# Performance work log

Measured on AMD Instinct MI355X. Metric: run time of the kernel, lower is better.

Reference implementation:

```python
import jax, jax.numpy as jnp
import numpy as np

N_NODES = 50000
N_EDGES = 1600000
IN_FEAT = 128
OUT_FEAT = 128
NUM_RELS = 16
NUM_BASES = 4


def setup_inputs() -> dict:
    key = jax.random.key(0)
    ks = jax.random.split(key, 7)
    x = jax.random.normal(ks[0], (N_NODES, IN_FEAT), dtype=jnp.float32)
    W_bases = jax.random.normal(ks[1], (NUM_BASES, IN_FEAT, OUT_FEAT), dtype=jnp.float32) * (1.0 / np.sqrt(IN_FEAT))
    w_comp = jax.random.normal(ks[2], (NUM_RELS, NUM_BASES), dtype=jnp.float32)
    norm = jax.random.uniform(ks[3], (N_EDGES, 1), dtype=jnp.float32)
    src = jax.random.randint(ks[4], (N_EDGES,), 0, N_NODES, dtype=jnp.int32)
    dst = jax.random.randint(ks[5], (N_EDGES,), 0, N_NODES, dtype=jnp.int32)
    etype = jax.random.randint(ks[6], (N_EDGES,), 0, NUM_RELS, dtype=jnp.int32)
    return {"x": x, "W_bases": W_bases, "w_comp": w_comp, "norm": norm,
            "src": src, "dst": dst, "etype": etype}


def _combine_weights(W_bases, w_comp):
    # Faithful to the torch code: stack -> permute(1,0,2) -> matmul -> view(-1, out) -> split(in_feat)
    # [B, in, out] -> [in, B, out]
    Wb = jnp.transpose(W_bases, (1, 0, 2))
    # [R, B] @ [in, B, out] (batched over 'in') -> [in, R, out]
    W = jnp.matmul(w_comp, Wb)
    # view(-1, out) then split into chunks of in_feat rows == reshape(R, in, out)
    return W.reshape(-1, OUT_FEAT).reshape(NUM_RELS, IN_FEAT, OUT_FEAT)


def reference(x, W_bases, w_comp, norm, src, dst, etype):
    # per-relation weights [R, in, out]
    W = _combine_weights(W_bases, w_comp)
    # src_mul_edge: gather source node features, scale by per-edge norm  [E, in]
    msg = x[src] * norm
    # 'sum' aggregation per (relation, dst-node) segment  -> [R, N, in]
    seg = etype.astype(jnp.int32) * N_NODES + dst.astype(jnp.int32)
    agg = jax.ops.segment_sum(msg, seg, num_segments=NUM_RELS * N_NODES)
    agg = agg.reshape(NUM_RELS, N_NODES, IN_FEAT)
    # per-relation mm then merge across relation subgraphs with node_reduce 'sum'  -> [N, out]
    out = jnp.einsum('rni,rio->no', agg, W)
    # bias=None, activation=None in this configuration
    return out
```

## Files before the change

kernel.cpp:

```cpp
#include <hip/hip_runtime.h>


#define N_NODES  50000
#define N_EDGES  1600000
#define IN_FEAT  128
#define OUT_FEAT 128
#define NUM_RELS 16
#define NUM_BASES 4
#define XC_K     32
#define BIN_CAP  96

#define OFF_CNT      0
#define OFF_SPILLCNT 200000
#define OFF_SPILL    200064
#define OFF_BINS     6600064
#define OFF_XC       45000064
#define WS_NEED      51400064

__global__ __launch_bounds__(256) void node_precomp(
    const float* __restrict__ x, const float* __restrict__ w_comp,
    float* __restrict__ xc)
{
  const int lane = threadIdx.x & 31;
  const int grp  = threadIdx.x >> 5;
  const int j = lane & 7;
  const int b = lane >> 3;

  float wc[16];
  #pragma unroll
  for (int t = 0; t < 16; ++t) wc[t] = w_comp[t * NUM_BASES + b];

  for (int n = blockIdx.x * 8 + grp; n < N_NODES; n += gridDim.x * 8) {
    const float4* xr = (const float4*)(x + (size_t)n * IN_FEAT) + j * 4;
    float acc = 0.f;
    #pragma unroll
    for (int q = 0; q < 4; ++q) {
      float4 v = xr[q];
      acc += v.x * wc[q*4+0] + v.y * wc[q*4+1]
           + v.z * wc[q*4+2] + v.w * wc[q*4+3];
    }
    xc[(size_t)n * XC_K + lane] = acc;
  }
}

__global__ __launch_bounds__(256) void bin_edges(
    const int* __restrict__ src, const int* __restrict__ dst,
    const int* __restrict__ etype, const float* __restrict__ norm,
    int* __restrict__ cnt, uint2* __restrict__ bins,
    int* __restrict__ spillcnt, int* __restrict__ spill)
{
  for (int e = blockIdx.x * blockDim.x + threadIdx.x; e < N_EDGES;
       e += gridDim.x * blockDim.x) {
    const int d  = dst[e];
    const int s  = src[e];
    const int et = etype[e];
    const float nm = norm[e];
    const int pos = atomicAdd(&cnt[d], 1);
    if (pos < BIN_CAP) {
      bins[(size_t)d * BIN_CAP + pos] =
          make_uint2((unsigned)s | ((unsigned)et << 17), __float_as_uint(nm));
    } else {
      const int k = atomicAdd(spillcnt, 1);
      if (k < N_EDGES) spill[k] = e;
    }
  }
}

__global__ __launch_bounds__(512) void rgcn_fused(
    const int* __restrict__ cnt, const uint2* __restrict__ bins,
    const float* __restrict__ xc, const float* __restrict__ Wb,
    float* __restrict__ out)
{
  __shared__ float acc[8 * 1024];

  const int t    = threadIdx.x;
  const int w    = t >> 6;
  const int lane = t & 63;
  const int h    = lane >> 5;
  const int l5   = lane & 31;
  const int jj4b = (l5 & 7) * 4 + (l5 >> 3);
  const int accBase = w * 1024 + h * 512;

  const int nodeBase = blockIdx.x * 8;
  const int n = nodeBase + w;

  #pragma unroll
  for (int q = 0; q < 4; ++q)
    *(float4*)&acc[w * 1024 + lane * 16 + q * 4] = make_float4(0.f,0.f,0.f,0.f);

  int cntv = 0;
  uint32_t B0x = 0, B0y = 0, B1x = 0, B1y = 0;
  if (n < N_NODES) {
    cntv = cnt[n]; if (cntv > BIN_CAP) cntv = BIN_CAP;
    const uint2* bp = bins + (size_t)n * BIN_CAP;
    uint2 v0 = bp[lane];  B0x = v0.x; B0y = v0.y;
    uint2 v1 = bp[(lane & 31) + 64]; B1x = v1.x; B1y = v1.y;
  }

  const int iters = (cntv + 1) >> 1;
  int   idx  = h;
  bool  act0 = idx < cntv;
  uint32_t wx = (idx < 64) ? __shfl(B0x, idx) : __shfl(B1x, (idx - 64) & 31);
  uint32_t wy = (idx < 64) ? __shfl(B0y, idx) : __shfl(B1y, (idx - 64) & 31);
  int   s0  = wx & 0x1FFFF;
  int   et0 = (wx >> 17) & 15;
  float nm0 = __uint_as_float(wy);
  float xc0 = act0 ? xc[(size_t)s0 * XC_K + l5] : 0.f;

  for (int i = 0; i < iters; ++i) {
    const int idx1 = 2 * (i + 1) + h;
    const bool act1 = idx1 < cntv;
    uint32_t nx = (idx1 < 64) ? __shfl(B0x, idx1) : __shfl(B1x, (idx1 - 64) & 31);
    uint32_t ny = (idx1 < 64) ? __shfl(B0y, idx1) : __shfl(B1y, (idx1 - 64) & 31);
    const int   s1  = nx & 0x1FFFF;
    const int   et1 = (nx >> 17) & 15;
    const float nm1 = __uint_as_float(ny);
    const float xc1 = act1 ? xc[(size_t)s1 * XC_K + l5] : 0.f;
    if (act0) {
      const int slot = accBase + et0 * 32 + jj4b;
      acc[slot] += xc0 * nm0;
    }
    act0 = act1; xc0 = xc1; et0 = et1; nm0 = nm1;
  }

  #pragma unroll
  for (int q = 0; q < 8; ++q) {
    const int idxm = w * 1024 + q * 64 + lane;
    acc[idxm] += acc[idxm + 512];
  }
  __syncthreads();

  const int o  = t & 127;
  const int g  = t >> 7;
  const float* a0p = &acc[(2 * g) * 1024];
  const float* a1p = &acc[(2 * g + 1) * 1024];
  const float* wp0 = Wb + o;
  float o0 = 0.f, o1 = 0.f;
  #pragma unroll 4
  for (int m = 0; m < 128; ++m) {
    const float4 a0 = *(const float4*)&a0p[m * 4];
    const float4 a1 = *(const float4*)&a1p[m * 4];
    const float w0 = wp0[(m          ) * 128];
    const float w1 = wp0[(m + 128    ) * 128];
    const float w2 = wp0[(m + 256    ) * 128];
    const float w3 = wp0[(m + 384    ) * 128];
    o0 += a0.x * w0 + a0.y * w1 + a0.z * w2 + a0.w * w3;
    o1 += a1.x * w0 + a1.y * w1 + a1.z * w2 + a1.w * w3;
  }
  const int n0 = nodeBase + 2 * g;
  const int n1 = n0 + 1;
  if (n0 < N_NODES) out[(size_t)n0 * OUT_FEAT + o] = o0;
  if (n1 < N_NODES) out[(size_t)n1 * OUT_FEAT + o] = o1;
}

__global__ __launch_bounds__(256) void spill_fix(
    const int* __restrict__ spillcnt, const int* __restrict__ spill,
    const float* __restrict__ xc, const float* __restrict__ Wb,
    const float* __restrict__ norm, const int* __restrict__ src,
    const int* __restrict__ dst, const int* __restrict__ etype,
    float* __restrict__ out)
{
  int cntv = *spillcnt; if (cntv > N_EDGES) cntv = N_EDGES;
  for (int idx = blockIdx.x * blockDim.x + threadIdx.x; idx < cntv;
       idx += gridDim.x * blockDim.x) {
    const int e = spill[idx];
    const int s = src[e], d = dst[e], et = etype[e];
    const float nm = norm[e];
    float m[32];
    #pragma unroll
    for (int l = 0; l < 32; ++l) m[l] = xc[(size_t)s * XC_K + l] * nm;
    for (int o = 0; o < OUT_FEAT; ++o) {
      float a = 0.f;
      #pragma unroll
      for (int l = 0; l < 32; ++l)
        a += m[l] * Wb[(size_t)((l >> 3) * 128 + et * 8 + (l & 7)) * OUT_FEAT + o];
      atomicAdd(&out[(size_t)d * OUT_FEAT + o], a);
    }
  }
}

__global__ __launch_bounds__(256) void edge_direct(
    const float* __restrict__ x, const float* __restrict__ W_bases,
    const float* __restrict__ w_comp, const float* __restrict__ norm,
    const int* __restrict__ src, const int* __restrict__ dst,
    const int* __restrict__ etype, float* __restrict__ out)
{
  const int wave = threadIdx.x >> 6;
  const int lane = threadIdx.x & 63;
  const int j = lane & 7;
  const int b = (lane >> 3) & 3;

  float wc[16];
  #pragma unroll
  for (int t = 0; t < 16; ++t) wc[t] = w_comp[t * NUM_BASES + b];

  for (int e = blockIdx.x * 4 + wave; e < N_EDGES; e += gridDim.x * 4) {
    const int   s  = src[e];
    const int   d  = dst[e];
    const int   et = etype[e];
    const float nm = norm[e];
    const float4* xr = (const float4*)(x + (size_t)s * IN_FEAT) + j * 4;
    float m = 0.f;
    #pragma unroll
    for (int q = 0; q < 4; ++q) {
      float4 v = xr[q];
      m += v.x * wc[q*4+0] + v.y * wc[q*4+1]
         + v.z * wc[q*4+2] + v.w * wc[q*4+3];
    }
    m *= nm;
    float acc0 = 0.f, acc1 = 0.f;
    #pragma unroll
    for (int p = 0; p < 32; ++p) {
      float mv = __shfl(m, p, 64);
      const float* Wr = W_bases + (size_t)((p >> 3) * 128 + et * 8 + (p & 7)) * OUT_FEAT;
      acc0 += mv * Wr[lane];
      acc1 += mv * Wr[64 + lane];
    }
    atomicAdd(out + (size_t)d * OUT_FEAT + lane, acc0);
    atomicAdd(out + (size_t)d * OUT_FEAT + 64 + lane, acc1);
  }
}

extern "C" void kernel_launch(void* const* d_in, const int* in_sizes, int n_in,
                              void* d_out, int out_size, void* d_ws, size_t ws_size,
                              hipStream_t stream) {
  const float* x       = (const float*)d_in[0];
  const float* W_bases = (const float*)d_in[1];
  const float* w_comp  = (const float*)d_in[2];
  const float* norm    = (const float*)d_in[3];
  const int*   src     = (const int*)d_in[4];
  const int*   dst     = (const int*)d_in[5];
  const int*   etype   = (const int*)d_in[6];
  float* out = (float*)d_out;

  if (ws_size >= (size_t)WS_NEED) {
    char* ws = (char*)d_ws;
    int*   cntp     = (int*)(ws + OFF_CNT);
    int*   spillcnt = (int*)(ws + OFF_SPILLCNT);
    int*   spill    = (int*)(ws + OFF_SPILL);
    uint2* bins     = (uint2*)(ws + OFF_BINS);
    float* xc       = (float*)(ws + OFF_XC);

    hipMemsetAsync(cntp, 0, 200064, stream);
    node_precomp<<<6250, 256, 0, stream>>>(x, w_comp, xc);
    bin_edges<<<6250, 256, 0, stream>>>(src, dst, etype, norm,
                                        cntp, bins, spillcnt, spill);
    rgcn_fused<<<(N_NODES + 7) / 8, 512, 0, stream>>>(cntp, bins, xc, W_bases, out);
    spill_fix<<<16, 256, 0, stream>>>(spillcnt, spill, xc, W_bases,
                                      norm, src, dst, etype, out);
  } else {
    hipMemsetAsync(out, 0, (size_t)out_size * sizeof(float), stream);
    edge_direct<<<8192, 256, 0, stream>>>(x, W_bases, w_comp, norm,
                                          src, dst, etype, out);
  }
}
```

Measured before the change: 461.2 us.

## Fuse prep kernels and register-tile the per-node weight GEMM in rgcn_fused

Merges node precompute and edge binning into one launch, with vectorized int4 loads for the edge arrays. The fused kernel now handles 16 nodes per block with LDS atomic accumulation and a transposed padded layout. The output GEMM is register-tiled (4 nodes by 8 outputs per thread, split-K across waves with an LDS tree reduction), so each W element is reused across nodes instead of reloaded per node. Risks include LDS atomic contention, extra barriers, and no bounds checks on nodes, which relies on N_NODES being divisible by 16.

```diff
diff --git a/kernel.cpp b/kernel.cpp
--- a/kernel.cpp
+++ b/kernel.cpp
@@ -9,6 +9,8 @@
 #define NUM_BASES 4
 #define XC_K     32
 #define BIN_CAP  96
+#define NPB      16
+#define ASTRIDE  20
 
 #define OFF_CNT      0
 #define OFF_SPILLCNT 200000
@@ -17,140 +19,190 @@
 #define OFF_XC       45000064
 #define WS_NEED      51400064
 
-__global__ __launch_bounds__(256) void node_precomp(
+__global__ __launch_bounds__(256) void prep(
     const float* __restrict__ x, const float* __restrict__ w_comp,
-    float* __restrict__ xc)
-{
-  const int lane = threadIdx.x & 31;
-  const int grp  = threadIdx.x >> 5;
-  const int j = lane & 7;
-  const int b = lane >> 3;
-
-  float wc[16];
-  #pragma unroll
-  for (int t = 0; t < 16; ++t) wc[t] = w_comp[t * NUM_BASES + b];
-
-  for (int n = blockIdx.x * 8 + grp; n < N_NODES; n += gridDim.x * 8) {
-    const float4* xr = (const float4*)(x + (size_t)n * IN_FEAT) + j * 4;
-    float acc = 0.f;
-    #pragma unroll
-    for (int q = 0; q < 4; ++q) {
-      float4 v = xr[q];
-      acc += v.x * wc[q*4+0] + v.y * wc[q*4+1]
-           + v.z * wc[q*4+2] + v.w * wc[q*4+3];
-    }
-    xc[(size_t)n * XC_K + lane] = acc;
-  }
-}
-
-__global__ __launch_bounds__(256) void bin_edges(
     const int* __restrict__ src, const int* __restrict__ dst,
     const int* __restrict__ etype, const float* __restrict__ norm,
-    int* __restrict__ cnt, uint2* __restrict__ bins,
+    float* __restrict__ xc, int* __restrict__ cnt, uint2* __restrict__ bins,
     int* __restrict__ spillcnt, int* __restrict__ spill)
 {
-  for (int e = blockIdx.x * blockDim.x + threadIdx.x; e < N_EDGES;
-       e += gridDim.x * blockDim.x) {
-    const int d  = dst[e];
-    const int s  = src[e];
-    const int et = etype[e];
-    const float nm = norm[e];
-    const int pos = atomicAdd(&cnt[d], 1);
-    if (pos < BIN_CAP) {
-      bins[(size_t)d * BIN_CAP + pos] =
-          make_uint2((unsigned)s | ((unsigned)et << 17), __float_as_uint(nm));
-    } else {
-      const int k = atomicAdd(spillcnt, 1);
-      if (k < N_EDGES) spill[k] = e;
-    }
-  }
-}
-
-__global__ __launch_bounds__(512) void rgcn_fused(
+  if (blockIdx.x < 512) {
+    const int lane = threadIdx.x & 31;
+    const int grp  = threadIdx.x >> 5;
+    const int j = lane & 7;
+    const int b = lane >> 3;
+    float wc[16];
+    #pragma unroll
+    for (int t = 0; t < 16; ++t) wc[t] = w_comp[t * NUM_BASES + b];
+    for (int n = blockIdx.x * 8 + grp; n < N_NODES; n += 512 * 8) {
+      const float4* xr = (const float4*)(x + (size_t)n * IN_FEAT) + j * 4;
+      float acc = 0.f;
+      #pragma unroll
+      for (int q = 0; q < 4; ++q) {
+        float4 v = xr[q];
+        acc += v.x * wc[q*4+0] + v.y * wc[q*4+1]
+             + v.z * wc[q*4+2] + v.w * wc[q*4+3];
+      }
+      xc[n * XC_K + lane] = acc;
+    }
+  } else {
+    const int bid = blockIdx.x - 512;
+    for (int e4 = (bid * 256 + threadIdx.x) * 4; e4 < N_EDGES;
+         e4 += 1536 * 256 * 4) {
+      const int4   s4 = *(const int4*)&src[e4];
+      const int4   d4 = *(const int4*)&dst[e4];
+      const int4   t4 = *(const int4*)&etype[e4];
+      const float4 n4 = *(const float4*)&norm[e4];
+      const int   ss[4] = {s4.x, s4.y, s4.z, s4.w};
+      const int   dd[4] = {d4.x, d4.y, d4.z, d4.w};
+      const int   tt[4] = {t4.x, t4.y, t4.z, t4.w};
+      const float nn[4] = {n4.x, n4.y, n4.z, n4.w};
+      #pragma unroll
+      for (int q = 0; q < 4; ++q) {
+        const int pos = atomicAdd(&cnt[dd[q]], 1);
+        if (pos < BIN_CAP) {
+          bins[(size_t)dd[q] * BIN_CAP + pos] =
+              make_uint2((unsigned)ss[q] | ((unsigned)tt[q] << 17),
+                         __float_as_uint(nn[q]));
+        } else {
+          const int k = atomicAdd(spillcnt, 1);
+          if (k < N_EDGES) spill[k] = e4 + q;
+        }
+      }
+    }
+  }
+}
+
+__device__ inline void red_write(float* accf, int slot, float4 (&ac)[4][2]) {
+  const int base = slot * 34;
+  #pragma unroll
+  for (int nn = 0; nn < 4; ++nn) {
+    *(float2*)&accf[base + nn*8 + 0] = make_float2(ac[nn][0].x, ac[nn][0].y);
+    *(float2*)&accf[base + nn*8 + 2] = make_float2(ac[nn][0].z, ac[nn][0].w);
+    *(float2*)&accf[base + nn*8 + 4] = make_float2(ac[nn][1].x, ac[nn][1].y);
+    *(float2*)&accf[base + nn*8 + 6] = make_float2(ac[nn][1].z, ac[nn][1].w);
+  }
+}
+__device__ inline void red_read(const float* accf, int slot, float4 (&ac)[4][2]) {
+  const int base = slot * 34;
+  #pragma unroll
+  for (int nn = 0; nn < 4; ++nn) {
+    float2 v0 = *(const float2*)&accf[base + nn*8 + 0];
+    float2 v1 = *(const float2*)&accf[base + nn*8 + 2];
+    float2 v2 = *(const float2*)&accf[base + nn*8 + 4];
+    float2 v3 = *(const float2*)&accf[base + nn*8 + 6];
+    ac[nn][0].x += v0.x; ac[nn][0].y += v0.y;
+    ac[nn][0].z += v1.x; ac[nn][0].w += v1.y;
+    ac[nn][1].x += v2.x; ac[nn][1].y += v2.y;
+    ac[nn][1].z += v3.x; ac[nn][1].w += v3.y;
+  }
+}
+
+__global__ __launch_bounds__(512, 4) void rgcn_fused(
     const int* __restrict__ cnt, const uint2* __restrict__ bins,
     const float* __restrict__ xc, const float* __restrict__ Wb,
     float* __restrict__ out)
 {
-  __shared__ float acc[8 * 1024];
+  __shared__ float accf[512 * ASTRIDE];
 
   const int t    = threadIdx.x;
   const int w    = t >> 6;
   const int lane = t & 63;
   const int h    = lane >> 5;
   const int l5   = lane & 31;
-  const int jj4b = (l5 & 7) * 4 + (l5 >> 3);
-  const int accBase = w * 1024 + h * 512;
-
-  const int nodeBase = blockIdx.x * 8;
-  const int n = nodeBase + w;
-
-  #pragma unroll
-  for (int q = 0; q < 4; ++q)
-    *(float4*)&acc[w * 1024 + lane * 16 + q * 4] = make_float4(0.f,0.f,0.f,0.f);
-
-  int cntv = 0;
-  uint32_t B0x = 0, B0y = 0, B1x = 0, B1y = 0;
-  if (n < N_NODES) {
-    cntv = cnt[n]; if (cntv > BIN_CAP) cntv = BIN_CAP;
-    const uint2* bp = bins + (size_t)n * BIN_CAP;
-    uint2 v0 = bp[lane];  B0x = v0.x; B0y = v0.y;
-    uint2 v1 = bp[(lane & 31) + 64]; B1x = v1.x; B1y = v1.y;
-  }
-
-  const int iters = (cntv + 1) >> 1;
-  int   idx  = h;
-  bool  act0 = idx < cntv;
-  uint32_t wx = (idx < 64) ? __shfl(B0x, idx) : __shfl(B1x, (idx - 64) & 31);
-  uint32_t wy = (idx < 64) ? __shfl(B0y, idx) : __shfl(B1y, (idx - 64) & 31);
-  int   s0  = wx & 0x1FFFF;
-  int   et0 = (wx >> 17) & 15;
-  float nm0 = __uint_as_float(wy);
-  float xc0 = act0 ? xc[(size_t)s0 * XC_K + l5] : 0.f;
-
-  for (int i = 0; i < iters; ++i) {
-    const int idx1 = 2 * (i + 1) + h;
-    const bool act1 = idx1 < cntv;
-    uint32_t nx = (idx1 < 64) ? __shfl(B0x, idx1) : __shfl(B1x, (idx1 - 64) & 31);
-    uint32_t ny = (idx1 < 64) ? __shfl(B0y, idx1) : __shfl(B1y, (idx1 - 64) & 31);
-    const int   s1  = nx & 0x1FFFF;
-    const int   et1 = (nx >> 17) & 15;
-    const float nm1 = __uint_as_float(ny);
-    const float xc1 = act1 ? xc[(size_t)s1 * XC_K + l5] : 0.f;
-    if (act0) {
-      const int slot = accBase + et0 * 32 + jj4b;
-      acc[slot] += xc0 * nm0;
-    }
-    act0 = act1; xc0 = xc1; et0 = et1; nm0 = nm1;
-  }
-
-  #pragma unroll
-  for (int q = 0; q < 8; ++q) {
-    const int idxm = w * 1024 + q * 64 + lane;
-    acc[idxm] += acc[idxm + 512];
-  }
-  __syncthreads();
-
-  const int o  = t & 127;
-  const int g  = t >> 7;
-  const float* a0p = &acc[(2 * g) * 1024];
-  const float* a1p = &acc[(2 * g + 1) * 1024];
-  const float* wp0 = Wb + o;
-  float o0 = 0.f, o1 = 0.f;
+  const int perm = (l5 & 7) * 4 + (l5 >> 3);
+
+  #pragma unroll
+  for (int i = 0; i < 5; ++i)
+    *(float4*)&accf[t * ASTRIDE + i * 4] = make_float4(0.f, 0.f, 0.f, 0.f);
+  __syncthreads();
+
+  const int nodeBase = blockIdx.x * NPB;
+  const int n0g = nodeBase + 2 * w;
+  const int n1g = n0g + 1;
+  int c0 = cnt[n0g]; if (c0 > BIN_CAP) c0 = BIN_CAP;
+  int c1 = cnt[n1g]; if (c1 > BIN_CAP) c1 = BIN_CAP;
+  const int tot = c0 + c1;
+
+  const uint2* bp0 = bins + (size_t)n0g * BIN_CAP;
+  const uint2* bp1 = bins + (size_t)n1g * BIN_CAP;
+  const int pb0 = perm * ASTRIDE + 2 * w;
+  const int pb1 = pb0 + 1;
+
+  uint2 bvA = make_uint2(0u, 0u), bvB = make_uint2(0u, 0u);
+  if (h < tot)     bvA = (h < c0)     ? bp0[h]            : bp1[h - c0];
+  if (h + 2 < tot) bvB = ((h+2) < c0) ? bp0[h+2]          : bp1[h+2-c0];
+  int   etA  = (bvA.x >> 17) & 15;
+  float nmA  = __uint_as_float(bvA.y);
+  int   selA = (h < c0) ? 0 : 1;
+  float xcA  = (h < tot) ? xc[(bvA.x & 0x1FFFF) * XC_K + l5] : 0.f;
+
+  for (int gi = h; gi < tot; gi += 2) {
+    const int gn = gi + 4;
+    uint2 bvC = make_uint2(0u, 0u);
+    if (gn < tot) bvC = (gn < c0) ? bp0[gn] : bp1[gn - c0];
+    const int gB = gi + 2;
+    const int   etB  = (bvB.x >> 17) & 15;
+    const float nmB  = __uint_as_float(bvB.y);
+    const int   selB = (gB < c0) ? 0 : 1;
+    const float xcB  = (gB < tot) ? xc[(bvB.x & 0x1FFFF) * XC_K + l5] : 0.f;
+    atomicAdd(&accf[etA * (32 * ASTRIDE) + (selA ? pb1 : pb0)], xcA * nmA);
+    bvB = bvC; etA = etB; nmA = nmB; xcA = xcB; selA = selB;
+  }
+  __syncthreads();
+
+  const int ks = w;
+  const int ng = lane & 3;
+  const int og = lane >> 2;
+  const float* wbase = Wb + og * 8;
+
+  float4 ac[4][2];
+  #pragma unroll
+  for (int nn = 0; nn < 4; ++nn) {
+    ac[nn][0] = make_float4(0.f, 0.f, 0.f, 0.f);
+    ac[nn][1] = make_float4(0.f, 0.f, 0.f, 0.f);
+  }
+
   #pragma unroll 4
-  for (int m = 0; m < 128; ++m) {
-    const float4 a0 = *(const float4*)&a0p[m * 4];
-    const float4 a1 = *(const float4*)&a1p[m * 4];
-    const float w0 = wp0[(m          ) * 128];
-    const float w1 = wp0[(m + 128    ) * 128];
-    const float w2 = wp0[(m + 256    ) * 128];
-    const float w3 = wp0[(m + 384    ) * 128];
-    o0 += a0.x * w0 + a0.y * w1 + a0.z * w2 + a0.w * w3;
-    o1 += a1.x * w0 + a1.y * w1 + a1.z * w2 + a1.w * w3;
-  }
-  const int n0 = nodeBase + 2 * g;
-  const int n1 = n0 + 1;
-  if (n0 < N_NODES) out[(size_t)n0 * OUT_FEAT + o] = o0;
-  if (n1 < N_NODES) out[(size_t)n1 * OUT_FEAT + o] = o1;
+  for (int q = 0; q < 64; ++q) {
+    const int ks2 = ks * 64 + q;
+    const int et = ks2 >> 5;
+    const int pj = (ks2 >> 2) & 7;
+    const int bb = ks2 & 3;
+    const int k2 = bb * 128 + et * 8 + pj;
+    const float4 a4 = *(const float4*)&accf[ks2 * ASTRIDE + ng * 4];
+    const float4 w0 = *(const float4*)&wbase[k2 * 128];
+    const float4 w1 = *(const float4*)&wbase[k2 * 128 + 4];
+    #pragma unroll
+    for (int nn = 0; nn < 4; ++nn) {
+      const float s = (nn == 0) ? a4.x : (nn == 1) ? a4.y : (nn == 2) ? a4.z : a4.w;
+      ac[nn][0].x += s * w0.x; ac[nn][0].y += s * w0.y;
+      ac[nn][0].z += s * w0.z; ac[nn][0].w += s * w0.w;
+      ac[nn][1].x += s * w1.x; ac[nn][1].y += s * w1.y;
+      ac[nn][1].z += s * w1.z; ac[nn][1].w += s * w1.w;
+    }
+  }
+
+  __syncthreads();
+  if (ks >= 4)             red_write(accf, (ks - 4) * 64 + lane, ac);
+  __syncthreads();
+  if (ks < 4)              red_read (accf, ks * 64 + lane, ac);
+  __syncthreads();
+  if (ks == 2 || ks == 3)  red_write(accf, (ks - 2) * 64 + lane, ac);
+  __syncthreads();
+  if (ks < 2)              red_read (accf, ks * 64 + lane, ac);
+  __syncthreads();
+  if (ks == 1)             red_write(accf, lane, ac);
+  __syncthreads();
+  if (ks == 0) {
+    red_read(accf, lane, ac);
+    #pragma unroll
+    for (int nn = 0; nn < 4; ++nn) {
+      const int node = nodeBase + ng * 4 + nn;
+      *(float4*)(out + (size_t)node * OUT_FEAT + og * 8)     = ac[nn][0];
+      *(float4*)(out + (size_t)node * OUT_FEAT + og * 8 + 4) = ac[nn][1];
+    }
+  }
 }
 
 __global__ __launch_bounds__(256) void spill_fix(
@@ -189,15 +241,11 @@
   const int lane = threadIdx.x & 63;
   const int j = lane & 7;
   const int b = (lane >> 3) & 3;
-
   float wc[16];
   #pragma unroll
   for (int t = 0; t < 16; ++t) wc[t] = w_comp[t * NUM_BASES + b];
-
   for (int e = blockIdx.x * 4 + wave; e < N_EDGES; e += gridDim.x * 4) {
-    const int   s  = src[e];
-    const int   d  = dst[e];
-    const int   et = etype[e];
+    const int s = src[e], d = dst[e], et = etype[e];
     const float nm = norm[e];
     const float4* xr = (const float4*)(x + (size_t)s * IN_FEAT) + j * 4;
     float m = 0.f;
@@ -242,10 +290,9 @@
     float* xc       = (float*)(ws + OFF_XC);
 
     hipMemsetAsync(cntp, 0, 200064, stream);
-    node_precomp<<<6250, 256, 0, stream>>>(x, w_comp, xc);
-    bin_edges<<<6250, 256, 0, stream>>>(src, dst, etype, norm,
-                                        cntp, bins, spillcnt, spill);
-    rgcn_fused<<<(N_NODES + 7) / 8, 512, 0, stream>>>(cntp, bins, xc, W_bases, out);
+    prep<<<2048, 256, 0, stream>>>(x, w_comp, src, dst, etype, norm,
+                                   xc, cntp, bins, spillcnt, spill);
+    rgcn_fused<<<N_NODES / NPB, 512, 0, stream>>>(cntp, bins, xc, W_bases, out);
     spill_fix<<<16, 256, 0, stream>>>(spillcnt, spill, xc, W_bases,
                                       norm, src, dst, etype, out);
   } else {
```

Result: slower. 490.4 us (+6.3%).
